# Kernel optimization log

Measured on AMD Instinct MI355X. Metric: run time of the kernel, lower is better.

## Reference

```python
import jax, jax.numpy as jnp
import numpy as np

N_QUBITS = 4
N_LAYERS = 3
N_FEATURES = 64
BATCH = 524288


def setup_inputs() -> dict:
    key = jax.random.key(0)
    k1, k2, k3, k4 = jax.random.split(key, 4)
    x = jax.random.normal(k1, (BATCH, N_FEATURES), jnp.float32)
    # nn.Linear(64, 4) params
    lim = 1.0 / np.sqrt(N_FEATURES)
    W_pre = jax.random.uniform(k2, (N_QUBITS, N_FEATURES), jnp.float32, -lim, lim)
    b_pre = jax.random.uniform(k3, (N_QUBITS,), jnp.float32, -lim, lim)
    # quantum circuit weights: randn * 0.1
    qweights = jax.random.normal(k4, (N_LAYERS, N_QUBITS, 2), jnp.float32) * 0.1
    return {"x": x, "W_pre": W_pre, "b_pre": b_pre, "qweights": qweights}


def _coef(theta, n):
    # reshape scalar or [B] angle to broadcast against [B, 2,..,2] (n-1 trailing dims after slicing)
    return jnp.reshape(theta, (-1,) + (1,) * (n - 1))


def _apply_ry(state, wire, theta):
    # RY(t) = [[cos t/2, -sin t/2], [sin t/2, cos t/2]] applied on `wire`
    n = state.ndim - 1
    s = jnp.moveaxis(state, 1 + wire, -1)
    a, b = s[..., 0], s[..., 1]
    c = _coef(jnp.cos(theta / 2), n)
    sn = _coef(jnp.sin(theta / 2), n)
    out = jnp.stack([c * a - sn * b, sn * a + c * b], axis=-1)
    return jnp.moveaxis(out, -1, 1 + wire)


def _apply_rz(state, wire, theta):
    # RZ(t) = diag(e^{-i t/2}, e^{+i t/2})
    n = state.ndim - 1
    s = jnp.moveaxis(state, 1 + wire, -1)
    half = _coef(theta / 2, n)
    out = jnp.stack([jnp.exp(-1j * half) * s[..., 0],
                     jnp.exp(1j * half) * s[..., 1]], axis=-1)
    return jnp.moveaxis(out, -1, 1 + wire)


def _apply_cnot(state, ctrl, tgt):
    s = jnp.moveaxis(state, (1 + ctrl, 1 + tgt), (-2, -1))
    s = jnp.concatenate([s[..., 0:1, :], s[..., 1:2, ::-1]], axis=-2)
    return jnp.moveaxis(s, (-2, -1), (1 + ctrl, 1 + tgt))


def _circuit(angles, qweights):
    # batched 4-qubit statevector simulation; state shape [B, 2,2,2,2] (wire 0 = MSB)
    B, n = angles.shape
    nl = qweights.shape[0]
    state = jnp.zeros((B,) + (2,) * n, jnp.complex64)
    state = state.at[(slice(None),) + (0,) * n].set(1.0)
    for w in range(n):
        state = _apply_ry(state, w, angles[:, w])
    for l in range(nl):
        for w in range(n):
            state = _apply_ry(state, w, qweights[l, w, 0])
            state = _apply_rz(state, w, qweights[l, w, 1])
        for w in range(n):
            state = _apply_cnot(state, w, (w + 1) % n)
    probs = state.real ** 2 + state.imag ** 2  # [B, 2,2,2,2] float32
    exps = []
    for w in range(n):
        marg = jnp.moveaxis(probs, 1 + w, 1).reshape(B, 2, -1).sum(-1)  # [B, 2]
        exps.append(marg[:, 0] - marg[:, 1])  # <Z_w>
    return jnp.stack(exps, axis=1)  # [B, n]


def reference(x, W_pre, b_pre, qweights):
    angles = jnp.tanh(x @ W_pre.T + b_pre)  # [B, n_qubits]
    return _circuit(angles, qweights).astype(jnp.float32)
```

## Files before the change

### kernel.cpp

```cpp
#include <hip/hip_runtime.h>
#include <hip/hip_bf16.h>
#include <cmath>


typedef __attribute__((ext_vector_type(8))) short bf16x8;
typedef __attribute__((ext_vector_type(4))) float f32x4;

__global__ __launch_bounds__(256) void qprep_kernel(
    const float* __restrict__ qw,
    float* __restrict__ A_out)
{
  __shared__ float sre[16][17];
  __shared__ float sim[16][17];
  __shared__ float M[4][16][16];
  const int tid = threadIdx.x;
  const int col = tid >> 4;
  const int u   = tid & 15;

  sre[col][u] = (u == col) ? 1.0f : 0.0f;
  sim[col][u] = 0.0f;
  __syncthreads();

#pragma unroll
  for (int l = 0; l < 3; ++l) {
#pragma unroll
    for (int w = 0; w < 4; ++w) {
      const int mask = 8 >> w;
      float sh, ch, sh2, ch2;
      __sincosf(0.5f * qw[(l * 4 + w) * 2 + 0], &sh, &ch);
      __sincosf(0.5f * qw[(l * 4 + w) * 2 + 1], &sh2, &ch2);
      const int ua = u & ~mask, ub = u | mask;
      const float ar = sre[col][ua], ai = sim[col][ua];
      const float br = sre[col][ub], bi = sim[col][ub];
      __syncthreads();
      float nr, ni;
      if (u & mask) { nr = sh * ar + ch * br; ni = sh * ai + ch * bi; }
      else          { nr = ch * ar - sh * br; ni = ch * ai - sh * bi; }
      float rr, ri;
      if (u & mask) { rr = ch2 * nr - sh2 * ni; ri = ch2 * ni + sh2 * nr; }
      else          { rr = ch2 * nr + sh2 * ni; ri = ch2 * ni - sh2 * nr; }
      sre[col][u] = rr; sim[col][u] = ri;
      __syncthreads();
    }
    int src = u;
    if (src & 1) src ^= 8;
    if (src & 2) src ^= 1;
    if (src & 4) src ^= 2;
    if (src & 8) src ^= 4;
    const float pr = sre[col][src], pi = sim[col][src];
    __syncthreads();
    sre[col][u] = pr; sim[col][u] = pi;
    __syncthreads();
  }

  for (int idx = tid; idx < 1024; idx += 256) {
    const int w = idx >> 8, s = (idx >> 4) & 15, t = idx & 15;
    const int mask = 8 >> w;
    float acc = 0.0f;
#pragma unroll
    for (int uu = 0; uu < 16; ++uu) {
      const float z = (uu & mask) ? -1.0f : 1.0f;
      acc += z * (sre[s][uu] * sre[t][uu] + sim[s][uu] * sim[t][uu]);
    }
    M[w][s][t] = acc;
  }
  __syncthreads();

  for (int idx = tid; idx < 324; idx += 256) {
    const int w = idx & 3, pq = idx >> 2;
    const int p = pq / 9, q = pq % 9;
    const int i0 = p / 3, i1 = p % 3, i2 = q / 3, i3 = q % 3;
    float acc = 0.0f;
#pragma unroll
    for (int comb = 0; comb < 16; ++comb) {
      int s = 0, t = 0;
      float coef = 0.0625f;
      int j;
      j = (comb >> 3) & 1; s |= j << 3; t |= ((i0 == 2) ? (j ^ 1) : j) << 3; if (i0 == 1 && j) coef = -coef;
      j = (comb >> 2) & 1; s |= j << 2; t |= ((i1 == 2) ? (j ^ 1) : j) << 2; if (i1 == 1 && j) coef = -coef;
      j = (comb >> 1) & 1; s |= j << 1; t |= ((i2 == 2) ? (j ^ 1) : j) << 1; if (i2 == 1 && j) coef = -coef;
      j = comb & 1;        s |= j;      t |= ((i3 == 2) ? (j ^ 1) : j);      if (i3 == 1 && j) coef = -coef;
      acc = fmaf(coef, M[w][s][t], acc);
    }
    A_out[idx] = acc;
  }
}

__device__ __forceinline__ bf16x8 pack8(const float4 va, const float4 vb) {
  union { bf16x8 v; __hip_bfloat16 h[8]; } u;
  u.h[0] = __float2bfloat16(va.x); u.h[1] = __float2bfloat16(va.y);
  u.h[2] = __float2bfloat16(va.z); u.h[3] = __float2bfloat16(va.w);
  u.h[4] = __float2bfloat16(vb.x); u.h[5] = __float2bfloat16(vb.y);
  u.h[6] = __float2bfloat16(vb.z); u.h[7] = __float2bfloat16(vb.w);
  return u.v;
}

__device__ __forceinline__ float ftanh(float a) {
  return 1.0f - 2.0f * __builtin_amdgcn_rcpf(__expf(2.0f * a) + 1.0f);
}

__device__ __forceinline__ void gll16(const float* g, float* l) {
  __builtin_amdgcn_global_load_lds(
      (const __attribute__((address_space(1))) void*)g,
      (__attribute__((address_space(3))) void*)l, 16, 0, 0);
}

#define STAGE(S) {                                                          \
  const float* gb_ = x + (wrow0 + (size_t)((S) * 16)) * 64;                 \
  float* lb_ = sb + ((S) & 1) * 1024;                                       \
  gll16(gb_ + (((0 * 256 + lane * 4) ^ ((((0 * 4) + (lane >> 4)) & 7) << 2))), lb_ + 0 * 256); \
  gll16(gb_ + (((1 * 256 + lane * 4) ^ ((((1 * 4) + (lane >> 4)) & 7) << 2))), lb_ + 1 * 256); \
  gll16(gb_ + (((2 * 256 + lane * 4) ^ ((((2 * 4) + (lane >> 4)) & 7) << 2))), lb_ + 2 * 256); \
  gll16(gb_ + (((3 * 256 + lane * 4) ^ ((((3 * 4) + (lane >> 4)) & 7) << 2))), lb_ + 3 * 256); }

#define VM(N) { asm volatile("s_waitcnt vmcnt(" #N ")" ::: "memory");       \
                __builtin_amdgcn_sched_barrier(0); }
#define LG0() { asm volatile("s_waitcnt lgkmcnt(0)" ::: "memory");          \
                __builtin_amdgcn_sched_barrier(0); }

#define CONSUME(S) {                                                        \
  const float* s_ = sb + ((S) & 1) * 1024;                                  \
  const float4 f0 = *reinterpret_cast<const float4*>(s_ + ((cb_ + 0) ^ rw_)); \
  const float4 f1 = *reinterpret_cast<const float4*>(s_ + ((cb_ + 4) ^ rw_)); \
  const float4 f2 = *reinterpret_cast<const float4*>(s_ + ((cb_ + 32) ^ rw_)); \
  const float4 f3 = *reinterpret_cast<const float4*>(s_ + ((cb_ + 36) ^ rw_)); \
  const bf16x8 af0_ = pack8(f0, f1);                                        \
  const bf16x8 af1_ = pack8(f2, f3);                                        \
  f32x4 acc_ = __builtin_amdgcn_mfma_f32_16x16x32_bf16(af0_, wf0, zero, 0, 0, 0); \
  acc_ = __builtin_amdgcn_mfma_f32_16x16x32_bf16(af1_, wf1, acc_, 0, 0, 0); \
  if (arow < 4) {                                                           \
    _Pragma("unroll")                                                       \
    for (int r_ = 0; r_ < 4; ++r_)                                          \
      ap[((((S) & 3) * 16) + kgrp * 4 + r_) * 4 + arow] = acc_[r_];         \
  } }

#define TAIL(R0) {                                                          \
  asm volatile("s_waitcnt lgkmcnt(0)" ::: "memory");                        \
  __builtin_amdgcn_sched_barrier(0);                                        \
  const float4 ang = *reinterpret_cast<const float4*>(&ap[lane * 4]);       \
  const float t0 = ftanh(ang.x + bp[0]);                                    \
  const float t1 = ftanh(ang.y + bp[1]);                                    \
  const float t2 = ftanh(ang.z + bp[2]);                                    \
  const float t3 = ftanh(ang.w + bp[3]);                                    \
  float c0, s0, c1, s1, c2, s2, c3, s3;                                     \
  __sincosf(t0, &s0, &c0); __sincosf(t1, &s1, &c1);                         \
  __sincosf(t2, &s2, &c2); __sincosf(t3, &s3, &c3);                         \
  const float g[9] = {1.f, c1, s1, c0, c0 * c1, c0 * s1,                    \
                      s0, s0 * c1, s0 * s1};                                \
  const float h[9] = {1.f, c3, s3, c2, c2 * c3, c2 * s3,                    \
                      s2, s2 * c3, s2 * s3};                                \
  float e0 = 0.f, e1 = 0.f, e2 = 0.f, e3 = 0.f;                             \
  _Pragma("unroll")                                                         \
  for (int p_ = 0; p_ < 9; ++p_) {                                          \
    _Pragma("unroll")                                                       \
    for (int q_ = 0; q_ < 9; ++q_) {                                        \
      const float4 a4 = Aws[p_ * 9 + q_];                                   \
      const float tt = g[p_] * h[q_];                                       \
      e0 = fmaf(a4.x, tt, e0); e1 = fmaf(a4.y, tt, e1);                     \
      e2 = fmaf(a4.z, tt, e2); e3 = fmaf(a4.w, tt, e3);                     \
    }                                                                       \
  }                                                                         \
  reinterpret_cast<float4*>(out)[(R0) + lane] =                             \
      make_float4(e0, e1, e2, e3);                                          \
  asm volatile("" ::: "memory"); }

__global__ __launch_bounds__(256)
__attribute__((amdgpu_waves_per_eu(4, 4)))
void qmain_kernel(
    const float* __restrict__ x,
    const float* __restrict__ Wp,
    const float* __restrict__ bp,
    const float4* __restrict__ Aws,
    float* __restrict__ out)
{
  __shared__ alignas(16) float lds[4 * 2304];

  const int tid  = threadIdx.x;
  const int lane = tid & 63;
  const int wid  = tid >> 6;
  const int arow = lane & 15;
  const int kgrp = lane >> 4;
  float* sb = &lds[wid * 2304];
  float* ap = sb + 2048;

  const size_t wrow0 = ((size_t)blockIdx.x * 4 + wid) * 128;
  const int rw_ = (arow & 7) << 2;
  const int cb_ = arow * 64 + kgrp * 8;

  bf16x8 wf0, wf1;
#pragma unroll
  for (int j = 0; j < 8; ++j) {
    if (arow < 4) {
      union { short s; __hip_bfloat16 h; } u0, u1;
      u0.h = __float2bfloat16(Wp[arow * 64 + 0  + kgrp * 8 + j]);
      u1.h = __float2bfloat16(Wp[arow * 64 + 32 + kgrp * 8 + j]);
      wf0[j] = u0.s; wf1[j] = u1.s;
    } else {
      wf0[j] = 0; wf1[j] = 0;
    }
  }
  const f32x4 zero = {0.f, 0.f, 0.f, 0.f};

  const size_t r0 = wrow0;
  const size_t r1 = wrow0 + 64;

  STAGE(0);
  STAGE(1);
  VM(4);  CONSUME(0);
  LG0();  STAGE(2);
  VM(4);  CONSUME(1);
  LG0();  STAGE(3);
  VM(4);  CONSUME(2);
  LG0();  STAGE(4);
  VM(4);  CONSUME(3);
  LG0();  STAGE(5);

  TAIL(r0);

  VM(5);  CONSUME(4);
  LG0();  STAGE(6);
  VM(5);  CONSUME(5);
  LG0();  STAGE(7);
  VM(4);  CONSUME(6);
  VM(0);  CONSUME(7);

  TAIL(r1);
}

extern "C" void kernel_launch(void* const* d_in, const int* in_sizes, int n_in,
                              void* d_out, int out_size, void* d_ws, size_t ws_size,
                              hipStream_t stream) {
  const float* x  = (const float*)d_in[0];
  const float* Wp = (const float*)d_in[1];
  const float* bp = (const float*)d_in[2];
  const float* qw = (const float*)d_in[3];
  float* out = (float*)d_out;
  float* A = (float*)d_ws;
  (void)n_in; (void)out_size; (void)ws_size;

  qprep_kernel<<<1, 256, 0, stream>>>(qw, A);

  const int B = in_sizes[0] / 64;
  qmain_kernel<<<B / 512, 256, 0, stream>>>(x, Wp, bp,
                                            (const float4*)A, out);
}
```

Before: 35.82 us.

## Drop double-buffered LDS pipeline for single-buffer, more waves per wave

Each wave now handles 64 rows instead of 128, with a single LDS staging buffer and a full vmcnt(0) wait before every consume instead of double-buffered prefetch. The LDS footprint shrinks and waves_per_eu rises from 4 to 6-8, with twice as many blocks launched. The aim is to hide memory latency through occupancy rather than software pipelining. The cost is that each wave stalls fully on every load and gives up the overlap of the next tile's load with the current one's compute.

```diff
diff --git a/kernel.cpp b/kernel.cpp
--- a/kernel.cpp
+++ b/kernel.cpp
@@ -107,23 +107,21 @@
 
 #define STAGE(S) {                                                          \
   const float* gb_ = x + (wrow0 + (size_t)((S) * 16)) * 64;                 \
-  float* lb_ = sb + ((S) & 1) * 1024;                                       \
-  gll16(gb_ + (((0 * 256 + lane * 4) ^ ((((0 * 4) + (lane >> 4)) & 7) << 2))), lb_ + 0 * 256); \
-  gll16(gb_ + (((1 * 256 + lane * 4) ^ ((((1 * 4) + (lane >> 4)) & 7) << 2))), lb_ + 1 * 256); \
-  gll16(gb_ + (((2 * 256 + lane * 4) ^ ((((2 * 4) + (lane >> 4)) & 7) << 2))), lb_ + 2 * 256); \
-  gll16(gb_ + (((3 * 256 + lane * 4) ^ ((((3 * 4) + (lane >> 4)) & 7) << 2))), lb_ + 3 * 256); }
-
-#define VM(N) { asm volatile("s_waitcnt vmcnt(" #N ")" ::: "memory");       \
+  gll16(gb_ + (((0 * 256 + lane * 4) ^ ((((0 * 4) + (lane >> 4)) & 7) << 2))), sb + 0 * 256); \
+  gll16(gb_ + (((1 * 256 + lane * 4) ^ ((((1 * 4) + (lane >> 4)) & 7) << 2))), sb + 1 * 256); \
+  gll16(gb_ + (((2 * 256 + lane * 4) ^ ((((2 * 4) + (lane >> 4)) & 7) << 2))), sb + 2 * 256); \
+  gll16(gb_ + (((3 * 256 + lane * 4) ^ ((((3 * 4) + (lane >> 4)) & 7) << 2))), sb + 3 * 256); }
+
+#define VM0() { asm volatile("s_waitcnt vmcnt(0)" ::: "memory");            \
                 __builtin_amdgcn_sched_barrier(0); }
 #define LG0() { asm volatile("s_waitcnt lgkmcnt(0)" ::: "memory");          \
                 __builtin_amdgcn_sched_barrier(0); }
 
 #define CONSUME(S) {                                                        \
-  const float* s_ = sb + ((S) & 1) * 1024;                                  \
-  const float4 f0 = *reinterpret_cast<const float4*>(s_ + ((cb_ + 0) ^ rw_)); \
-  const float4 f1 = *reinterpret_cast<const float4*>(s_ + ((cb_ + 4) ^ rw_)); \
-  const float4 f2 = *reinterpret_cast<const float4*>(s_ + ((cb_ + 32) ^ rw_)); \
-  const float4 f3 = *reinterpret_cast<const float4*>(s_ + ((cb_ + 36) ^ rw_)); \
+  const float4 f0 = *reinterpret_cast<const float4*>(sb + ((cb_ + 0) ^ rw_)); \
+  const float4 f1 = *reinterpret_cast<const float4*>(sb + ((cb_ + 4) ^ rw_)); \
+  const float4 f2 = *reinterpret_cast<const float4*>(sb + ((cb_ + 32) ^ rw_)); \
+  const float4 f3 = *reinterpret_cast<const float4*>(sb + ((cb_ + 36) ^ rw_)); \
   const bf16x8 af0_ = pack8(f0, f1);                                        \
   const bf16x8 af1_ = pack8(f2, f3);                                        \
   f32x4 acc_ = __builtin_amdgcn_mfma_f32_16x16x32_bf16(af0_, wf0, zero, 0, 0, 0); \
@@ -131,41 +129,11 @@
   if (arow < 4) {                                                           \
     _Pragma("unroll")                                                       \
     for (int r_ = 0; r_ < 4; ++r_)                                          \
-      ap[((((S) & 3) * 16) + kgrp * 4 + r_) * 4 + arow] = acc_[r_];         \
+      ap[((S) * 16 + kgrp * 4 + r_) * 4 + arow] = acc_[r_];                 \
   } }
 
-#define TAIL(R0) {                                                          \
-  asm volatile("s_waitcnt lgkmcnt(0)" ::: "memory");                        \
-  __builtin_amdgcn_sched_barrier(0);                                        \
-  const float4 ang = *reinterpret_cast<const float4*>(&ap[lane * 4]);       \
-  const float t0 = ftanh(ang.x + bp[0]);                                    \
-  const float t1 = ftanh(ang.y + bp[1]);                                    \
-  const float t2 = ftanh(ang.z + bp[2]);                                    \
-  const float t3 = ftanh(ang.w + bp[3]);                                    \
-  float c0, s0, c1, s1, c2, s2, c3, s3;                                     \
-  __sincosf(t0, &s0, &c0); __sincosf(t1, &s1, &c1);                         \
-  __sincosf(t2, &s2, &c2); __sincosf(t3, &s3, &c3);                         \
-  const float g[9] = {1.f, c1, s1, c0, c0 * c1, c0 * s1,                    \
-                      s0, s0 * c1, s0 * s1};                                \
-  const float h[9] = {1.f, c3, s3, c2, c2 * c3, c2 * s3,                    \
-                      s2, s2 * c3, s2 * s3};                                \
-  float e0 = 0.f, e1 = 0.f, e2 = 0.f, e3 = 0.f;                             \
-  _Pragma("unroll")                                                         \
-  for (int p_ = 0; p_ < 9; ++p_) {                                          \
-    _Pragma("unroll")                                                       \
-    for (int q_ = 0; q_ < 9; ++q_) {                                        \
-      const float4 a4 = Aws[p_ * 9 + q_];                                   \
-      const float tt = g[p_] * h[q_];                                       \
-      e0 = fmaf(a4.x, tt, e0); e1 = fmaf(a4.y, tt, e1);                     \
-      e2 = fmaf(a4.z, tt, e2); e3 = fmaf(a4.w, tt, e3);                     \
-    }                                                                       \
-  }                                                                         \
-  reinterpret_cast<float4*>(out)[(R0) + lane] =                             \
-      make_float4(e0, e1, e2, e3);                                          \
-  asm volatile("" ::: "memory"); }
-
 __global__ __launch_bounds__(256)
-__attribute__((amdgpu_waves_per_eu(4, 4)))
+__attribute__((amdgpu_waves_per_eu(6, 8)))
 void qmain_kernel(
     const float* __restrict__ x,
     const float* __restrict__ Wp,
@@ -173,17 +141,17 @@
     const float4* __restrict__ Aws,
     float* __restrict__ out)
 {
-  __shared__ alignas(16) float lds[4 * 2304];
+  __shared__ alignas(16) float lds[4 * 1280];
 
   const int tid  = threadIdx.x;
   const int lane = tid & 63;
   const int wid  = tid >> 6;
   const int arow = lane & 15;
   const int kgrp = lane >> 4;
-  float* sb = &lds[wid * 2304];
-  float* ap = sb + 2048;
-
-  const size_t wrow0 = ((size_t)blockIdx.x * 4 + wid) * 128;
+  float* sb = &lds[wid * 1280];
+  float* ap = sb + 1024;
+
+  const size_t wrow0 = ((size_t)blockIdx.x * 4 + wid) * 64;
   const int rw_ = (arow & 7) << 2;
   const int cb_ = arow * 64 + kgrp * 8;
 
@@ -201,30 +169,37 @@
   }
   const f32x4 zero = {0.f, 0.f, 0.f, 0.f};
 
-  const size_t r0 = wrow0;
-  const size_t r1 = wrow0 + 64;
-
-  STAGE(0);
-  STAGE(1);
-  VM(4);  CONSUME(0);
-  LG0();  STAGE(2);
-  VM(4);  CONSUME(1);
-  LG0();  STAGE(3);
-  VM(4);  CONSUME(2);
-  LG0();  STAGE(4);
-  VM(4);  CONSUME(3);
-  LG0();  STAGE(5);
-
-  TAIL(r0);
-
-  VM(5);  CONSUME(4);
-  LG0();  STAGE(6);
-  VM(5);  CONSUME(5);
-  LG0();  STAGE(7);
-  VM(4);  CONSUME(6);
-  VM(0);  CONSUME(7);
-
-  TAIL(r1);
+  STAGE(0); VM0(); CONSUME(0);
+  LG0(); STAGE(1); VM0(); CONSUME(1);
+  LG0(); STAGE(2); VM0(); CONSUME(2);
+  LG0(); STAGE(3); VM0(); CONSUME(3);
+
+  LG0();
+  const float4 ang = *reinterpret_cast<const float4*>(&ap[lane * 4]);
+  const float t0 = ftanh(ang.x + bp[0]);
+  const float t1 = ftanh(ang.y + bp[1]);
+  const float t2 = ftanh(ang.z + bp[2]);
+  const float t3 = ftanh(ang.w + bp[3]);
+
+  float c0, s0, c1, s1, c2, s2, c3, s3;
+  __sincosf(t0, &s0, &c0); __sincosf(t1, &s1, &c1);
+  __sincosf(t2, &s2, &c2); __sincosf(t3, &s3, &c3);
+
+  const float g[9] = {1.f, c1, s1, c0, c0 * c1, c0 * s1, s0, s0 * c1, s0 * s1};
+  const float h[9] = {1.f, c3, s3, c2, c2 * c3, c2 * s3, s2, s2 * c3, s2 * s3};
+
+  float e0 = 0.f, e1 = 0.f, e2 = 0.f, e3 = 0.f;
+#pragma unroll
+  for (int p = 0; p < 9; ++p) {
+#pragma unroll
+    for (int q = 0; q < 9; ++q) {
+      const float4 a4 = Aws[p * 9 + q];
+      const float tt = g[p] * h[q];
+      e0 = fmaf(a4.x, tt, e0); e1 = fmaf(a4.y, tt, e1);
+      e2 = fmaf(a4.z, tt, e2); e3 = fmaf(a4.w, tt, e3);
+    }
+  }
+  reinterpret_cast<float4*>(out)[wrow0 + lane] = make_float4(e0, e1, e2, e3);
 }
 
 extern "C" void kernel_launch(void* const* d_in, const int* in_sizes, int n_in,
@@ -241,6 +216,6 @@
   qprep_kernel<<<1, 256, 0, stream>>>(qw, A);
 
   const int B = in_sizes[0] / 64;
-  qmain_kernel<<<B / 512, 256, 0, stream>>>(x, Wp, bp,
+  qmain_kernel<<<B / 256, 256, 0, stream>>>(x, Wp, bp,
                                             (const float4*)A, out);
 }
```

New measurement: 37.07 us. 1.03x slower.
